# Optimization experiments

Hardware: AMD Instinct MI355X
Metric: run time of the kernel (lower is better)

Reference implementation:

```python
import jax, jax.numpy as jnp
import numpy as np

T, B, K, N, M = 1024, 32, 8, 64, 64
DELTA = 3  # number of passes: DELTA-1 states-only + 1 final with output


def setup_inputs():
    key = jax.random.key(0)
    ks = jax.random.split(key, 7)
    x = jax.random.normal(ks[0], (T, B, K), jnp.float32)
    # stable, a.s.-distinct complex eigenvalues: |lam| in [0.5, 0.99)
    mag = jax.random.uniform(ks[1], (K, N), jnp.float32, 0.5, 0.99)
    phase = jax.random.uniform(ks[2], (K, N), jnp.float32, -np.pi, np.pi)
    lam_re = mag * jnp.cos(phase)
    lam_im = mag * jnp.sin(phase)
    C_re = jax.random.normal(ks[3], (K, N, M), jnp.float32) / np.sqrt(N)
    C_im = jax.random.normal(ks[4], (K, N, M), jnp.float32) / np.sqrt(N)
    D = jax.random.normal(ks[5], (K, M), jnp.float32)
    Do = jax.random.normal(ks[6], (K, M), jnp.float32)
    return {"x": x, "lam_re": lam_re, "lam_im": lam_im,
            "C_re": C_re, "C_im": C_im, "D": D, "Do": Do}


def _compute_Bp(lam):
    # Bʹ[k,j] = exp(-sum_i log(1 - lam_i/lam_j)), diagonal ratio zeroed
    k, n = lam.shape
    ratios = lam[:, :, None] / lam[:, None, :]           # (k, n, n)
    eye = jnp.eye(n, dtype=bool)[None]
    ratios = jnp.where(eye, jnp.zeros((), ratios.dtype), ratios)
    lnBp = -jnp.sum(jnp.log(1.0 - ratios), axis=1)       # (k, n)
    return jnp.exp(lnBp)


def _linear_recurrence(a, bx):
    # s_t = a_t * s_{t-1} + bx_t, computed as a parallel associative scan
    def comb(l, r):
        al, bl = l
        ar, br = r
        return (al * ar, bl * ar + br)
    _, s = jax.lax.associative_scan(comb, (a, bx), axis=0)
    return s


def _states(xc, lam, Bp, alpha):
    # one pass of the complex diagonal SSM; returns states (T, B, K, N)
    Bpx = (xc[..., None] * Bp).reshape(T, B, K * N)       # Bʹ·x
    if alpha is None:
        al = jnp.broadcast_to(lam.reshape(1, 1, K * N), (T, B, K * N))
    else:
        al = (alpha * lam[None, None]).reshape(T, B, K * N)  # α·λ
    # standard=True: shift inputs by one step (prepend zeros, drop last)
    z = jnp.zeros((1, B, K * N), al.dtype)
    al = jnp.concatenate([z, al[:-1]], axis=0)
    Bpx = jnp.concatenate([z, Bpx[:-1]], axis=0)
    return _linear_recurrence(al, Bpx).reshape(T, B, K, N)


def _forward(x, lam_re, lam_im, C_re, C_im, D, Do):
    lam = (lam_re + 1j * lam_im).astype(jnp.complex64)    # (K, N)
    Cp = (C_re + 1j * C_im).astype(jnp.complex64)         # (K, N, M)
    xc = x.astype(jnp.complex64)                          # (T, B, K)
    Bp = _compute_Bp(lam)                                 # (K, N)

    alpha = None
    for _ in range(DELTA - 1):
        s = _states(xc, lam, Bp, alpha)                   # (T, B, K, N)
        ls = lam[None, None] * s                          # λ·sʹ
        alpha = 1.0 / jnp.sqrt(1.0 + ls * jnp.conj(ls))   # recipsq

    s = _states(xc, lam, Bp, alpha)                       # final pass
    Cs = jnp.einsum("tbkn,knm->tbkm", s, Cp)              # Cʹ·sʹ
    Dx = xc[..., None] * D.astype(jnp.complex64)          # D·x
    y = Cs + Dx + Do.astype(jnp.complex64)                # (T, B, K, M)
    return jnp.mean(y, axis=2)                            # average over k


def reference(x, lam_re, lam_im, C_re, C_im, D, Do):
    return _forward(x, lam_re, lam_im, C_re, C_im, D, Do)
```

## Files before the change

kernel.cpp:

```cpp
#include <hip/hip_runtime.h>

#define TT 1024
#define BB 32
#define KKD 8
#define NN 64
#define MM 64
#define BKC (BB*KKD)
#define KN  (KKD*NN)

typedef __attribute__((ext_vector_type(8))) _Float16 f16x8;
typedef __attribute__((ext_vector_type(2))) __fp16 fp16x2;
typedef __attribute__((ext_vector_type(4))) float f32x4;

#define SC_DOWN (1.0f/4096.0f)
#define SC_UP   512.0f


static __device__ __forceinline__ float bcast(float v, int lane) {
    return __builtin_bit_cast(float,
        __builtin_amdgcn_readlane(__builtin_bit_cast(int, v), lane));
}
static __device__ __forceinline__ float f16lo(unsigned int pk) {
    return (float)__builtin_bit_cast(_Float16, (unsigned short)(pk & 0xffffu));
}
static __device__ __forceinline__ float f16hi(unsigned int pk) {
    return (float)__builtin_bit_cast(_Float16, (unsigned short)(pk >> 16));
}

__global__ __launch_bounds__(64) void bp_kernel(const float* __restrict__ lam_re,
                                                const float* __restrict__ lam_im,
                                                float* __restrict__ bp) {
    int k = blockIdx.x;
    int j = threadIdx.x;
    double ljre = (double)lam_re[k*NN+j], ljim = (double)lam_im[k*NN+j];
    double dj = ljre*ljre + ljim*ljim;
    double pre = 1.0, pim = 0.0;
    for (int i = 0; i < NN; ++i) {
        if (i == j) continue;
        double lire = (double)lam_re[k*NN+i], liim = (double)lam_im[k*NN+i];
        double rre = (lire*ljre + liim*ljim)/dj;
        double rim = (liim*ljre - lire*ljim)/dj;
        double zre = 1.0 - rre, zim = -rim;
        double zd = zre*zre + zim*zim;
        double npre = (pre*zre + pim*zim)/zd;
        double npim = (pim*zre - pre*zim)/zd;
        pre = npre; pim = npim;
    }
    bp[(k*NN+j)*2+0] = (float)pre;
    bp[(k*NN+j)*2+1] = (float)pim;
}

__global__ __launch_bounds__(256) void wprep_kernel(const float* __restrict__ C_re,
                                                    const float* __restrict__ C_im,
                                                    unsigned short* __restrict__ Wt) {
    int idx = blockIdx.x*256 + threadIdx.x;
    int m  = idx >> 10;
    int j  = idx & 1023;
    int kn = j >> 1;
    float v = (j & 1) ? -C_im[kn*MM + m] : C_re[kn*MM + m];
    Wt[idx] = __builtin_bit_cast(unsigned short, (_Float16)(v * SC_UP));
}

__global__ __launch_bounds__(512, 8) void scan_par4_kernel(const float* __restrict__ x,
                                                           const float* __restrict__ lam_re,
                                                           const float* __restrict__ lam_im,
                                                           const float* __restrict__ bp,
                                                           unsigned int* __restrict__ abuf,
                                                           int TL) {
    __shared__ float e1[32][16][2];
    __shared__ float e2[32][16][2];
    __shared__ float e3[32][16][2];
    __shared__ float pa2[32][16];
    __shared__ float pa3[32][16];
    __shared__ unsigned int apk[32][16][17];

    int blk = blockIdx.x;
    int bk = blk >> 2;
    int q2 = blk & 3;
    int b = bk >> 3;
    int k = bk & 7;
    int tid = threadIdx.x;
    int seg = tid >> 4;
    int nl  = tid & 15;
    int n   = q2*16 + nl;
    int kn  = k*NN + n;

    float lre = lam_re[kn], lim = lam_im[kn];
    float bpre = bp[2*kn+0], bpim = bp[2*kn+1];
    float l2 = lre*lre + lim*lim;

    float p32re = lre, p32im = lim;
    #pragma unroll
    for (int i = 0; i < 5; ++i) {
        float tr = p32re*p32re - p32im*p32im;
        float ti = 2.f*p32re*p32im;
        p32re = tr; p32im = ti;
    }

    float xs0 = x[(size_t)(seg*32 + nl)*BKC + b*KKD + k];
    float xs1 = x[(size_t)(seg*32 + 16 + nl)*BKC + b*KKD + k];

    float s1re = 0.f, s1im = 0.f;
    #pragma unroll
    for (int i = 0; i < 32; ++i) {
        float xv = (i < 16) ? __shfl(xs0, i, 16) : __shfl(xs1, i - 16, 16);
        float ure = xv*bpre, uim = xv*bpim;
        float tre = __builtin_fmaf(lre, s1re, __builtin_fmaf(-lim, s1im, ure));
        float tim = __builtin_fmaf(lre, s1im, __builtin_fmaf( lim, s1re, uim));
        s1re = tre; s1im = tim;
    }
    e1[seg][nl][0] = s1re; e1[seg][nl][1] = s1im;
    __syncthreads();
    float c1re = 0.f, c1im = 0.f;
    for (int i = 0; i < seg; ++i) {
        float tre = __builtin_fmaf(p32re, c1re, __builtin_fmaf(-p32im, c1im, e1[i][nl][0]));
        float tim = __builtin_fmaf(p32re, c1im, __builtin_fmaf( p32im, c1re, e1[i][nl][1]));
        c1re = tre; c1im = tim;
    }

    s1re = c1re; s1im = c1im;
    float s2re = 0.f, s2im = 0.f, pa = 1.f;
    float a1prev = 0.f;
    #pragma unroll
    for (int i = 0; i < 32; ++i) {
        float xv = (i < 16) ? __shfl(xs0, i, 16) : __shfl(xs1, i - 16, 16);
        float ure = xv*bpre, uim = xv*bpim;
        float mm1 = __builtin_fmaf(l2, __builtin_fmaf(s1re, s1re, s1im*s1im), 1.f);
        float a1 = rsqrtf(mm1);
        float t1re = __builtin_fmaf(lre, s1re, __builtin_fmaf(-lim, s1im, ure));
        float t1im = __builtin_fmaf(lre, s1im, __builtin_fmaf( lim, s1re, uim));
        s1re = t1re; s1im = t1im;
        float cr = a1*lre, ci = a1*lim;
        float t2re = __builtin_fmaf(cr, s2re, __builtin_fmaf(-ci, s2im, ure));
        float t2im = __builtin_fmaf(cr, s2im, __builtin_fmaf( ci, s2re, uim));
        s2re = t2re; s2im = t2im;
        pa *= a1;
        if (i & 1)
            apk[seg][i>>1][nl] = __builtin_bit_cast(unsigned int,
                                   __builtin_amdgcn_cvt_pkrtz(a1prev, a1));
        else
            a1prev = a1;
    }
    e2[seg][nl][0] = s2re; e2[seg][nl][1] = s2im; pa2[seg][nl] = pa;
    __syncthreads();
    float c2re = 0.f, c2im = 0.f;
    for (int i = 0; i < seg; ++i) {
        float pai = pa2[i][nl];
        float qre = pai*p32re, qim = pai*p32im;
        float tre = __builtin_fmaf(qre, c2re, __builtin_fmaf(-qim, c2im, e2[i][nl][0]));
        float tim = __builtin_fmaf(qre, c2im, __builtin_fmaf( qim, c2re, e2[i][nl][1]));
        c2re = tre; c2im = tim;
    }

    s2re = c2re; s2im = c2im;
    float s3re = 0.f, s3im = 0.f, pb = 1.f;
    float a2prev = 0.f;
    unsigned int pk = 0;
    #pragma unroll
    for (int i = 0; i < 32; ++i) {
        if (!(i & 1)) pk = apk[seg][i>>1][nl];
        float a1 = (i & 1) ? f16hi(pk) : f16lo(pk);
        float xv = (i < 16) ? __shfl(xs0, i, 16) : __shfl(xs1, i - 16, 16);
        float ure = xv*bpre, uim = xv*bpim;
        float mm2 = __builtin_fmaf(l2, __builtin_fmaf(s2re, s2re, s2im*s2im), 1.f);
        float a2 = rsqrtf(mm2);
        float cr = a1*lre, ci = a1*lim;
        float t2re = __builtin_fmaf(cr, s2re, __builtin_fmaf(-ci, s2im, ure));
        float t2im = __builtin_fmaf(cr, s2im, __builtin_fmaf( ci, s2re, uim));
        s2re = t2re; s2im = t2im;
        float dr = a2*lre, di = a2*lim;
        float t3re = __builtin_fmaf(dr, s3re, __builtin_fmaf(-di, s3im, ure));
        float t3im = __builtin_fmaf(dr, s3im, __builtin_fmaf( di, s3re, uim));
        s3re = t3re; s3im = t3im;
        pb *= a2;
        if (i & 1)
            apk[seg][i>>1][nl] = __builtin_bit_cast(unsigned int,
                                   __builtin_amdgcn_cvt_pkrtz(a2prev, a2));
        else
            a2prev = a2;
    }
    e3[seg][nl][0] = s3re; e3[seg][nl][1] = s3im; pa3[seg][nl] = pb;
    __syncthreads();
    float c3re = 0.f, c3im = 0.f;
    for (int i = 0; i < seg; ++i) {
        float pbi = pa3[i][nl];
        float qre = pbi*p32re, qim = pbi*p32im;
        float tre = __builtin_fmaf(qre, c3re, __builtin_fmaf(-qim, c3im, e3[i][nl][0]));
        float tim = __builtin_fmaf(qre, c3im, __builtin_fmaf( qim, c3re, e3[i][nl][1]));
        c3re = tre; c3im = tim;
    }

    s3re = c3re; s3im = c3im;
    unsigned int* ap = abuf + (size_t)(bk*4 + q2)*((size_t)TL*16)
                     + (seg >> 2)*2048 + (seg & 3)*16 + nl;
    #pragma unroll
    for (int i = 0; i < 32; ++i) {
        fp16x2 hv = __builtin_amdgcn_cvt_pkrtz(s3re*SC_DOWN, s3im*SC_DOWN);
        ap[(size_t)i * 64] = __builtin_bit_cast(unsigned int, hv);
        if (!(i & 1)) pk = apk[seg][i>>1][nl];
        float a2 = (i & 1) ? f16hi(pk) : f16lo(pk);
        float xv = (i < 16) ? __shfl(xs0, i, 16) : __shfl(xs1, i - 16, 16);
        float ure = xv*bpre, uim = xv*bpim;
        float dr = a2*lre, di = a2*lim;
        float t3re = __builtin_fmaf(dr, s3re, __builtin_fmaf(-di, s3im, ure));
        float t3im = __builtin_fmaf(dr, s3im, __builtin_fmaf( di, s3re, uim));
        s3re = t3re; s3im = t3im;
    }
}

__global__ __launch_bounds__(64) void scan_seq_kernel(const float* __restrict__ x,
                                                      const float* __restrict__ lam_re,
                                                      const float* __restrict__ lam_im,
                                                      const float* __restrict__ bp,
                                                      float* __restrict__ state,
                                                      unsigned int* __restrict__ abuf,
                                                      int chunk_start, int chunk_len,
                                                      int TL) {
    int bk = blockIdx.x;
    int b = bk >> 3;
    int k = bk & 7;
    int n = threadIdx.x;
    int kn = k*NN + n;
    float lre = lam_re[kn], lim = lam_im[kn];
    float bpre = bp[2*kn+0], bpim = bp[2*kn+1];
    float l2 = lre*lre + lim*lim;
    int chain = bk*NN + n;

    float s1re,s1im,s2re,s2im,s3re,s3im;
    if (chunk_start == 0) {
        s1re=s1im=s2re=s2im=s3re=s3im=0.f;
    } else {
        const float* st = state + (size_t)chain*6;
        s1re=st[0];s1im=st[1];s2re=st[2];s2im=st[3];s3re=st[4];s3im=st[5];
    }

    const float* xp = x + (size_t)chunk_start*BKC + b*KKD + k;
    int q2_ = n >> 4, nl_ = n & 15;
    unsigned int* ab = abuf + (size_t)(bk*4 + q2_)*((size_t)TL*16) + nl_;

    float xs = xp[(size_t)n * BKC];
    for (int t0 = 0; t0 < chunk_len; t0 += 64) {
        float xs_nxt = 0.f;
        if (t0 + 64 < chunk_len) xs_nxt = xp[(size_t)(t0 + 64 + n) * BKC];
        #pragma unroll
        for (int w = 0; w < 4; ++w) {
            float mm_[16], cre[16], cim[16];
            #pragma unroll
            for (int j = 0; j < 16; ++j) {
                float xv = bcast(xs, w*16 + j);
                mm_[j] = __builtin_fmaf(l2, s1re*s1re + s1im*s1im, 1.0f);
                float ure = xv*bpre, uim = xv*bpim;
                float tre = __builtin_fmaf(lre, s1re, __builtin_fmaf(-lim, s1im, ure));
                float tim = __builtin_fmaf(lre, s1im, __builtin_fmaf( lim, s1re, uim));
                s1re=tre; s1im=tim;
            }
            #pragma unroll
            for (int j = 0; j < 16; ++j) {
                float a = rsqrtf(mm_[j]); cre[j] = a*lre; cim[j] = a*lim;
            }
            #pragma unroll
            for (int j = 0; j < 16; ++j) {
                float xv = bcast(xs, w*16 + j);
                mm_[j] = __builtin_fmaf(l2, s2re*s2re + s2im*s2im, 1.0f);
                float ure = xv*bpre, uim = xv*bpim;
                float tre = __builtin_fmaf(cre[j], s2re, __builtin_fmaf(-cim[j], s2im, ure));
                float tim = __builtin_fmaf(cre[j], s2im, __builtin_fmaf( cim[j], s2re, uim));
                s2re=tre; s2im=tim;
            }
            #pragma unroll
            for (int j = 0; j < 16; ++j) {
                float a = rsqrtf(mm_[j]); cre[j] = a*lre; cim[j] = a*lim;
            }
            #pragma unroll
            for (int j = 0; j < 16; ++j) {
                int t = t0 + w*16 + j;
                fp16x2 hv = __builtin_amdgcn_cvt_pkrtz(s3re*SC_DOWN, s3im*SC_DOWN);
                ab[((size_t)(t >> 7))*2048 + (t & 31)*64 + ((t >> 5) & 3)*16]
                    = __builtin_bit_cast(unsigned int, hv);
                float xv = bcast(xs, w*16 + j);
                float ure = xv*bpre, uim = xv*bpim;
                float tre = __builtin_fmaf(cre[j], s3re, __builtin_fmaf(-cim[j], s3im, ure));
                float tim = __builtin_fmaf(cre[j], s3im, __builtin_fmaf( cim[j], s3re, uim));
                s3re=tre; s3im=tim;
            }
        }
        xs = xs_nxt;
    }
    float* st = state + (size_t)chain*6;
    st[0]=s1re;st[1]=s1im;st[2]=s2re;st[3]=s2im;st[4]=s3re;st[5]=s3im;
}

__global__ __launch_bounds__(256) void proj_kernel(const unsigned int* __restrict__ A,
                                                   const unsigned short* __restrict__ Wt,
                                                   const float* __restrict__ x,
                                                   const float* __restrict__ D,
                                                   const float* __restrict__ Do,
                                                   float* __restrict__ out,
                                                   int rowOff, int TL) {
    __shared__ uint4 At[2][1024];
    __shared__ uint4 Wb[2][1024];
    int tid = threadIdx.x;
    int w = tid >> 6, l = tid & 63;
    int lg = l >> 4, lr = l & 15;
    int wr = w >> 1, wc = w & 1;
    int bI = blockIdx.x;
    int R0 = bI * 64;
    size_t TLQ = (size_t)TL * 16;

    f32x4 acc[2][2];
    #pragma unroll
    for (int g = 0; g < 2; ++g)
        #pragma unroll
        for (int t = 0; t < 2; ++t) acc[g][t] = (f32x4){0.f,0.f,0.f,0.f};

    uint4 ra[4], rw[4];
    int srow[4], su[4];
    #pragma unroll
    for (int i = 0; i < 4; ++i) {
        int unit = w*256 + i*64 + l;
        srow[i] = unit >> 4;
        su[i]   = unit & 15;
    }

    #pragma unroll
    for (int i = 0; i < 4; ++i) {
        int row = srow[i], u = su[i];
        int b = row & 31, t2 = (bI << 1) + (row >> 5);
        size_t idx = (size_t)((b*8 + 0)*4 + (u >> 2))*TLQ
                   + (size_t)(t2 >> 7)*2048 + (t2 & 31)*64 + ((t2 >> 5) & 3)*16 + (u & 3)*4;
        ra[i] = *(const uint4*)(A + idx);
        rw[i] = *(const uint4*)((const char*)Wt + (row*2048 + 0*256 + u*16));
    }
    #pragma unroll
    for (int i = 0; i < 4; ++i) {
        int row = srow[i], u = su[i];
        At[0][row*16 + (u ^ (row & 7))] = ra[i];
        Wb[0][row*16 + (u ^ (row & 7))] = rw[i];
    }
    __syncthreads();

    for (int kc = 0; kc < 8; ++kc) {
        int cur = kc & 1;
        if (kc < 7) {
            int kn = kc + 1;
            #pragma unroll
            for (int i = 0; i < 4; ++i) {
                int row = srow[i], u = su[i];
                int b = row & 31, t2 = (bI << 1) + (row >> 5);
                size_t idx = (size_t)((b*8 + kn)*4 + (u >> 2))*TLQ
                           + (size_t)(t2 >> 7)*2048 + (t2 & 31)*64 + ((t2 >> 5) & 3)*16 + (u & 3)*4;
                ra[i] = *(const uint4*)(A + idx);
                rw[i] = *(const uint4*)((const char*)Wt + (row*2048 + kn*256 + u*16));
            }
        }
        #pragma unroll
        for (int ks = 0; ks < 4; ++ks) {
            f16x8 af[2], bf[2];
            #pragma unroll
            for (int g = 0; g < 2; ++g) {
                int row = (wr*2 + g)*16 + lr;
                af[g] = __builtin_bit_cast(f16x8, At[cur][row*16 + ((ks*4 + lg) ^ (row & 7))]);
            }
            #pragma unroll
            for (int t = 0; t < 2; ++t) {
                int m = (wc*2 + t)*16 + lr;
                bf[t] = __builtin_bit_cast(f16x8, Wb[cur][m*16 + ((ks*4 + lg) ^ (m & 7))]);
            }
            #pragma unroll
            for (int g = 0; g < 2; ++g)
                #pragma unroll
                for (int t = 0; t < 2; ++t)
                    acc[g][t] = __builtin_amdgcn_mfma_f32_16x16x32_f16(af[g], bf[t], acc[g][t], 0,0,0);
        }
        if (kc < 7) {
            int nb = (kc + 1) & 1;
            #pragma unroll
            for (int i = 0; i < 4; ++i) {
                int row = srow[i], u = su[i];
                At[nb][row*16 + (u ^ (row & 7))] = ra[i];
                Wb[nb][row*16 + (u ^ (row & 7))] = rw[i];
            }
        }
        __syncthreads();
    }

    #pragma unroll
    for (int g = 0; g < 2; ++g) {
        int rowA = rowOff + R0 + (wr*2 + g)*16 + lr;
        const float* xr = x + (size_t)rowA * KKD;
        float4 x0 = *(const float4*)(xr);
        float4 x1 = *(const float4*)(xr + 4);
        f16x8 a2;
        a2[0] = (lg==0) ? (_Float16)x0.x : ((lg==1) ? (_Float16)1.0f : (_Float16)0.0f);
        a2[1] = (lg==0) ? (_Float16)x0.y : (_Float16)0.0f;
        a2[2] = (lg==0) ? (_Float16)x0.z : (_Float16)0.0f;
        a2[3] = (lg==0) ? (_Float16)x0.w : (_Float16)0.0f;
        a2[4] = (lg==0) ? (_Float16)x1.x : (_Float16)0.0f;
        a2[5] = (lg==0) ? (_Float16)x1.y : (_Float16)0.0f;
        a2[6] = (lg==0) ? (_Float16)x1.z : (_Float16)0.0f;
        a2[7] = (lg==0) ? (_Float16)x1.w : (_Float16)0.0f;
        #pragma unroll
        for (int t = 0; t < 2; ++t) {
            int c = (wc*2 + t)*16 + lr;
            float dob = 0.f;
            #pragma unroll
            for (int i = 0; i < 8; ++i) dob += Do[i*64 + c];
            f16x8 b2;
            b2[0] = (lg==0) ? (_Float16)(D[0*64+c]*0.125f)
                  : ((lg==1) ? (_Float16)(dob*0.125f) : (_Float16)0.0f);
            b2[1] = (lg==0) ? (_Float16)(D[1*64+c]*0.125f) : (_Float16)0.0f;
            b2[2] = (lg==0) ? (_Float16)(D[2*64+c]*0.125f) : (_Float16)0.0f;
            b2[3] = (lg==0) ? (_Float16)(D[3*64+c]*0.125f) : (_Float16)0.0f;
            b2[4] = (lg==0) ? (_Float16)(D[4*64+c]*0.125f) : (_Float16)0.0f;
            b2[5] = (lg==0) ? (_Float16)(D[5*64+c]*0.125f) : (_Float16)0.0f;
            b2[6] = (lg==0) ? (_Float16)(D[6*64+c]*0.125f) : (_Float16)0.0f;
            b2[7] = (lg==0) ? (_Float16)(D[7*64+c]*0.125f) : (_Float16)0.0f;
            acc[g][t] = __builtin_amdgcn_mfma_f32_16x16x32_f16(a2, b2, acc[g][t], 0,0,0);
        }
    }

    #pragma unroll
    for (int g = 0; g < 2; ++g)
        #pragma unroll
        for (int t = 0; t < 2; ++t) {
            int c = (wc*2 + t)*16 + lr;
            #pragma unroll
            for (int reg = 0; reg < 4; ++reg) {
                int row = rowOff + R0 + (wr*2 + g)*16 + lg*4 + reg;
                out[(size_t)row*MM + c] = acc[g][t][reg];
            }
        }
}

extern "C" void kernel_launch(void* const* d_in, const int* in_sizes, int n_in,
                              void* d_out, int out_size, void* d_ws, size_t ws_size,
                              hipStream_t stream) {
    const float* x      = (const float*)d_in[0];
    const float* lam_re = (const float*)d_in[1];
    const float* lam_im = (const float*)d_in[2];
    const float* C_re   = (const float*)d_in[3];
    const float* C_im   = (const float*)d_in[4];
    const float* D      = (const float*)d_in[5];
    const float* Do     = (const float*)d_in[6];
    float* out = (float*)d_out;

    char* ws = (char*)d_ws;
    float*          bpw    = (float*)(ws);
    unsigned short* Wt     = (unsigned short*)(ws + 4096);
    float*          statew = (float*)(ws + 135168);
    unsigned int*   abuf   = (unsigned int*)(ws + 528384);

    bp_kernel<<<KKD, NN, 0, stream>>>(lam_re, lam_im, bpw);
    wprep_kernel<<<256, 256, 0, stream>>>(C_re, C_im, Wt);

    const size_t base = 528384;
    const size_t perT = (size_t)BB*KN*4;

    if (ws_size >= base + (size_t)TT*perT) {
        scan_par4_kernel<<<BKC*4, 512, 0, stream>>>(x, lam_re, lam_im, bpw, abuf, TT);
        proj_kernel<<<TT*BB/64, 256, 0, stream>>>(abuf, Wt, x, D, Do, out, 0, TT);
    } else {
        size_t avail = ws_size > base ? ws_size - base : 0;
        int chunkT = (int)(avail / perT) & ~127;
        if (chunkT < 128) chunkT = 128;
        for (int cs = 0; cs < TT; cs += chunkT) {
            int len = (chunkT < TT - cs) ? chunkT : (TT - cs);
            scan_seq_kernel<<<BKC, NN, 0, stream>>>(x, lam_re, lam_im, bpw, statew,
                                                    abuf, cs, len, len);
            proj_kernel<<<len*BB/64, 256, 0, stream>>>(abuf, Wt, x, D, Do, out,
                                                       cs*BB, len);
        }
    }
}
```

Before: 76.88 us.

## Halve projection tile rows and read weights directly from global in fragment layout

The projection GEMM now handles 32 rows per block instead of 64, which doubles the grid to one block per timestep and halves the A-staging shared memory. The weight matrix is pre-permuted by wprep into MFMA fragment order, so each lane loads its B fragment straight from global/L2 and the shared-memory weight buffer is gone. This raises parallelism and occupancy and removes LDS traffic for W. The cost is that every block now re-reads W from cache, and each block has less reuse per tile.

```diff
diff --git a/kernel.cpp b/kernel.cpp
--- a/kernel.cpp
+++ b/kernel.cpp
@@ -55,10 +55,12 @@
                                                     unsigned short* __restrict__ Wt) {
     int idx = blockIdx.x*256 + threadIdx.x;
     int m  = idx >> 10;
-    int j  = idx & 1023;
-    int kn = j >> 1;
-    float v = (j & 1) ? -C_im[kn*MM + m] : C_re[kn*MM + m];
-    Wt[idx] = __builtin_bit_cast(unsigned short, (_Float16)(v * SC_UP));
+    int c  = idx & 1023;
+    int kn = c >> 1;
+    float v = (c & 1) ? -C_im[kn*MM + m] : C_re[kn*MM + m];
+    int kc = c >> 7, ks = (c >> 5) & 3, lg = (c >> 3) & 3, e = c & 7;
+    int idx2 = (((kc*4 + ks)*4 + lg)*64 + m)*8 + e;
+    Wt[idx2] = __builtin_bit_cast(unsigned short, (_Float16)(v * SC_UP));
 }
 
 __global__ __launch_bounds__(512, 8) void scan_par4_kernel(const float* __restrict__ x,
@@ -297,139 +299,119 @@
                                                    const float* __restrict__ Do,
                                                    float* __restrict__ out,
                                                    int rowOff, int TL) {
-    __shared__ uint4 At[2][1024];
-    __shared__ uint4 Wb[2][1024];
+    __shared__ uint4 At[2][512];
     int tid = threadIdx.x;
     int w = tid >> 6, l = tid & 63;
     int lg = l >> 4, lr = l & 15;
     int wr = w >> 1, wc = w & 1;
     int bI = blockIdx.x;
-    int R0 = bI * 64;
+    int R0 = bI * 32;
     size_t TLQ = (size_t)TL * 16;
-
-    f32x4 acc[2][2];
-    #pragma unroll
-    for (int g = 0; g < 2; ++g)
-        #pragma unroll
-        for (int t = 0; t < 2; ++t) acc[g][t] = (f32x4){0.f,0.f,0.f,0.f};
-
-    uint4 ra[4], rw[4];
-    int srow[4], su[4];
-    #pragma unroll
-    for (int i = 0; i < 4; ++i) {
-        int unit = w*256 + i*64 + l;
+    int toff = (bI >> 7)*2048 + (bI & 31)*64 + ((bI >> 5) & 3)*16;
+
+    f32x4 acc[2];
+    acc[0] = (f32x4){0.f,0.f,0.f,0.f};
+    acc[1] = (f32x4){0.f,0.f,0.f,0.f};
+
+    uint4 ra[2];
+    int srow[2], su[2];
+    #pragma unroll
+    for (int i = 0; i < 2; ++i) {
+        int unit = i*256 + tid;
         srow[i] = unit >> 4;
         su[i]   = unit & 15;
     }
 
     #pragma unroll
-    for (int i = 0; i < 4; ++i) {
+    for (int i = 0; i < 2; ++i) {
         int row = srow[i], u = su[i];
-        int b = row & 31, t2 = (bI << 1) + (row >> 5);
-        size_t idx = (size_t)((b*8 + 0)*4 + (u >> 2))*TLQ
-                   + (size_t)(t2 >> 7)*2048 + (t2 & 31)*64 + ((t2 >> 5) & 3)*16 + (u & 3)*4;
+        size_t idx = (size_t)((row*8 + 0)*4 + (u >> 2))*TLQ + toff + (u & 3)*4;
         ra[i] = *(const uint4*)(A + idx);
-        rw[i] = *(const uint4*)((const char*)Wt + (row*2048 + 0*256 + u*16));
-    }
-    #pragma unroll
-    for (int i = 0; i < 4; ++i) {
+    }
+    #pragma unroll
+    for (int i = 0; i < 2; ++i) {
         int row = srow[i], u = su[i];
         At[0][row*16 + (u ^ (row & 7))] = ra[i];
-        Wb[0][row*16 + (u ^ (row & 7))] = rw[i];
     }
     __syncthreads();
 
+    int arow = wr*16 + lr;
     for (int kc = 0; kc < 8; ++kc) {
         int cur = kc & 1;
         if (kc < 7) {
             int kn = kc + 1;
             #pragma unroll
-            for (int i = 0; i < 4; ++i) {
+            for (int i = 0; i < 2; ++i) {
                 int row = srow[i], u = su[i];
-                int b = row & 31, t2 = (bI << 1) + (row >> 5);
-                size_t idx = (size_t)((b*8 + kn)*4 + (u >> 2))*TLQ
-                           + (size_t)(t2 >> 7)*2048 + (t2 & 31)*64 + ((t2 >> 5) & 3)*16 + (u & 3)*4;
+                size_t idx = (size_t)((row*8 + kn)*4 + (u >> 2))*TLQ + toff + (u & 3)*4;
                 ra[i] = *(const uint4*)(A + idx);
-                rw[i] = *(const uint4*)((const char*)Wt + (row*2048 + kn*256 + u*16));
             }
         }
         #pragma unroll
         for (int ks = 0; ks < 4; ++ks) {
-            f16x8 af[2], bf[2];
-            #pragma unroll
-            for (int g = 0; g < 2; ++g) {
-                int row = (wr*2 + g)*16 + lr;
-                af[g] = __builtin_bit_cast(f16x8, At[cur][row*16 + ((ks*4 + lg) ^ (row & 7))]);
-            }
+            f16x8 af = __builtin_bit_cast(f16x8,
+                At[cur][arow*16 + ((ks*4 + lg) ^ (arow & 7))]);
             #pragma unroll
             for (int t = 0; t < 2; ++t) {
-                int m = (wc*2 + t)*16 + lr;
-                bf[t] = __builtin_bit_cast(f16x8, Wb[cur][m*16 + ((ks*4 + lg) ^ (m & 7))]);
-            }
-            #pragma unroll
-            for (int g = 0; g < 2; ++g)
-                #pragma unroll
-                for (int t = 0; t < 2; ++t)
-                    acc[g][t] = __builtin_amdgcn_mfma_f32_16x16x32_f16(af[g], bf[t], acc[g][t], 0,0,0);
+                int m = wc*32 + t*16 + lr;
+                const unsigned short* bp_ = Wt + (size_t)(((kc*4 + ks)*4 + lg)*64 + m)*8;
+                f16x8 bf = __builtin_bit_cast(f16x8, *(const uint4*)bp_);
+                acc[t] = __builtin_amdgcn_mfma_f32_16x16x32_f16(af, bf, acc[t], 0,0,0);
+            }
         }
         if (kc < 7) {
             int nb = (kc + 1) & 1;
             #pragma unroll
-            for (int i = 0; i < 4; ++i) {
+            for (int i = 0; i < 2; ++i) {
                 int row = srow[i], u = su[i];
                 At[nb][row*16 + (u ^ (row & 7))] = ra[i];
-                Wb[nb][row*16 + (u ^ (row & 7))] = rw[i];
             }
         }
         __syncthreads();
     }
 
-    #pragma unroll
-    for (int g = 0; g < 2; ++g) {
-        int rowA = rowOff + R0 + (wr*2 + g)*16 + lr;
-        const float* xr = x + (size_t)rowA * KKD;
-        float4 x0 = *(const float4*)(xr);
-        float4 x1 = *(const float4*)(xr + 4);
-        f16x8 a2;
-        a2[0] = (lg==0) ? (_Float16)x0.x : ((lg==1) ? (_Float16)1.0f : (_Float16)0.0f);
-        a2[1] = (lg==0) ? (_Float16)x0.y : (_Float16)0.0f;
-        a2[2] = (lg==0) ? (_Float16)x0.z : (_Float16)0.0f;
-        a2[3] = (lg==0) ? (_Float16)x0.w : (_Float16)0.0f;
-        a2[4] = (lg==0) ? (_Float16)x1.x : (_Float16)0.0f;
-        a2[5] = (lg==0) ? (_Float16)x1.y : (_Float16)0.0f;
-        a2[6] = (lg==0) ? (_Float16)x1.z : (_Float16)0.0f;
-        a2[7] = (lg==0) ? (_Float16)x1.w : (_Float16)0.0f;
+    int rowA = rowOff + R0 + wr*16 + lr;
+    const float* xr = x + (size_t)rowA * KKD;
+    float4 x0 = *(const float4*)(xr);
+    float4 x1 = *(const float4*)(xr + 4);
+    f16x8 a2;
+    a2[0] = (lg==0) ? (_Float16)x0.x : ((lg==1) ? (_Float16)1.0f : (_Float16)0.0f);
+    a2[1] = (lg==0) ? (_Float16)x0.y : (_Float16)0.0f;
+    a2[2] = (lg==0) ? (_Float16)x0.z : (_Float16)0.0f;
+    a2[3] = (lg==0) ? (_Float16)x0.w : (_Float16)0.0f;
+    a2[4] = (lg==0) ? (_Float16)x1.x : (_Float16)0.0f;
+    a2[5] = (lg==0) ? (_Float16)x1.y : (_Float16)0.0f;
+    a2[6] = (lg==0) ? (_Float16)x1.z : (_Float16)0.0f;
+    a2[7] = (lg==0) ? (_Float16)x1.w : (_Float16)0.0f;
+
+    #pragma unroll
+    for (int t = 0; t < 2; ++t) {
+        int c = wc*32 + t*16 + lr;
+        float dob = 0.f;
         #pragma unroll
-        for (int t = 0; t < 2; ++t) {
-            int c = (wc*2 + t)*16 + lr;
-            float dob = 0.f;
-            #pragma unroll
-            for (int i = 0; i < 8; ++i) dob += Do[i*64 + c];
-            f16x8 b2;
-            b2[0] = (lg==0) ? (_Float16)(D[0*64+c]*0.125f)
-                  : ((lg==1) ? (_Float16)(dob*0.125f) : (_Float16)0.0f);
-            b2[1] = (lg==0) ? (_Float16)(D[1*64+c]*0.125f) : (_Float16)0.0f;
-            b2[2] = (lg==0) ? (_Float16)(D[2*64+c]*0.125f) : (_Float16)0.0f;
-            b2[3] = (lg==0) ? (_Float16)(D[3*64+c]*0.125f) : (_Float16)0.0f;
-            b2[4] = (lg==0) ? (_Float16)(D[4*64+c]*0.125f) : (_Float16)0.0f;
-            b2[5] = (lg==0) ? (_Float16)(D[5*64+c]*0.125f) : (_Float16)0.0f;
-            b2[6] = (lg==0) ? (_Float16)(D[6*64+c]*0.125f) : (_Float16)0.0f;
-            b2[7] = (lg==0) ? (_Float16)(D[7*64+c]*0.125f) : (_Float16)0.0f;
-            acc[g][t] = __builtin_amdgcn_mfma_f32_16x16x32_f16(a2, b2, acc[g][t], 0,0,0);
-        }
-    }
-
-    #pragma unroll
-    for (int g = 0; g < 2; ++g)
+        for (int i = 0; i < 8; ++i) dob += Do[i*64 + c];
+        f16x8 b2;
+        b2[0] = (lg==0) ? (_Float16)(D[0*64+c]*0.125f)
+              : ((lg==1) ? (_Float16)(dob*0.125f) : (_Float16)0.0f);
+        b2[1] = (lg==0) ? (_Float16)(D[1*64+c]*0.125f) : (_Float16)0.0f;
+        b2[2] = (lg==0) ? (_Float16)(D[2*64+c]*0.125f) : (_Float16)0.0f;
+        b2[3] = (lg==0) ? (_Float16)(D[3*64+c]*0.125f) : (_Float16)0.0f;
+        b2[4] = (lg==0) ? (_Float16)(D[4*64+c]*0.125f) : (_Float16)0.0f;
+        b2[5] = (lg==0) ? (_Float16)(D[5*64+c]*0.125f) : (_Float16)0.0f;
+        b2[6] = (lg==0) ? (_Float16)(D[6*64+c]*0.125f) : (_Float16)0.0f;
+        b2[7] = (lg==0) ? (_Float16)(D[7*64+c]*0.125f) : (_Float16)0.0f;
+        acc[t] = __builtin_amdgcn_mfma_f32_16x16x32_f16(a2, b2, acc[t], 0,0,0);
+    }
+
+    #pragma unroll
+    for (int t = 0; t < 2; ++t) {
+        int c = wc*32 + t*16 + lr;
         #pragma unroll
-        for (int t = 0; t < 2; ++t) {
-            int c = (wc*2 + t)*16 + lr;
-            #pragma unroll
-            for (int reg = 0; reg < 4; ++reg) {
-                int row = rowOff + R0 + (wr*2 + g)*16 + lg*4 + reg;
-                out[(size_t)row*MM + c] = acc[g][t][reg];
-            }
-        }
+        for (int reg = 0; reg < 4; ++reg) {
+            int row = rowOff + R0 + wr*16 + lg*4 + reg;
+            out[(size_t)row*MM + c] = acc[t][reg];
+        }
+    }
 }
 
 extern "C" void kernel_launch(void* const* d_in, const int* in_sizes, int n_in,
@@ -458,7 +440,7 @@
 
     if (ws_size >= base + (size_t)TT*perT) {
         scan_par4_kernel<<<BKC*4, 512, 0, stream>>>(x, lam_re, lam_im, bpw, abuf, TT);
-        proj_kernel<<<TT*BB/64, 256, 0, stream>>>(abuf, Wt, x, D, Do, out, 0, TT);
+        proj_kernel<<<TT, 256, 0, stream>>>(abuf, Wt, x, D, Do, out, 0, TT);
     } else {
         size_t avail = ws_size > base ? ws_size - base : 0;
         int chunkT = (int)(avail / perT) & ~127;
@@ -467,8 +449,8 @@
             int len = (chunkT < TT - cs) ? chunkT : (TT - cs);
             scan_seq_kernel<<<BKC, NN, 0, stream>>>(x, lam_re, lam_im, bpw, statew,
                                                     abuf, cs, len, len);
-            proj_kernel<<<len*BB/64, 256, 0, stream>>>(abuf, Wt, x, D, Do, out,
-                                                       cs*BB, len);
-        }
-    }
-}
+            proj_kernel<<<len, 256, 0, stream>>>(abuf, Wt, x, D, Do, out,
+                                                 cs*BB, len);
+        }
+    }
+}
```

Result: slower. 78.55 us (+2.2%).
